# Kernel optimization log

Hardware: AMD Instinct MI355X
Metric: run time of the kernel (lower is better)

The kernel has to match this reference:

```python
import jax, jax.numpy as jnp
import numpy as np

B, T, H, IN, OUT, HORIZON = 65536, 15, 128, 6, 3, 10
LN_EPS = 1e-5


def _w(k, shape, s=0.08):
    return jax.random.normal(k, shape, jnp.float32) * s


def setup_inputs() -> dict:
    key = jax.random.key(0)
    ks = jax.random.split(key, 16)
    return {
        "x": jax.random.normal(ks[0], (B, T, IN), jnp.float32),
        # encoder layer 0 (input 6 -> 128), PyTorch LSTM gate order i,f,g,o
        "W_ih0": _w(ks[1], (4 * H, IN)), "W_hh0": _w(ks[2], (4 * H, H)), "b0": jnp.zeros((4 * H,), jnp.float32),
        # encoder layer 1 (128 -> 128)
        "W_ih1": _w(ks[3], (4 * H, H)), "W_hh1": _w(ks[4], (4 * H, H)), "b1": jnp.zeros((4 * H,), jnp.float32),
        # decoder LSTM (128 -> 128)
        "W_ihd": _w(ks[5], (4 * H, H)), "W_hhd": _w(ks[6], (4 * H, H)), "bd": jnp.zeros((4 * H,), jnp.float32),
        # step embedding [pred_horizon+1, H]
        "emb": _w(ks[7], (HORIZON + 1, H), 0.5),
        # decoder_input_proj: Linear(3+128 -> 128)
        "Wp": _w(ks[8], (H, OUT + H)), "bp": jnp.zeros((H,), jnp.float32),
        # heads
        "Wm": _w(ks[9], (OUT, H)), "bm": jnp.zeros((OUT,), jnp.float32),
        "Ws": _w(ks[10], (OUT, H)), "bs": jnp.zeros((OUT,), jnp.float32),
        # dec_ln
        "ln_g": jnp.ones((H,), jnp.float32), "ln_b": jnp.zeros((H,), jnp.float32),
    }


def _lstm_cell(h, c, x_t, Wih, Whh, b):
    g = x_t @ Wih.T + h @ Whh.T + b  # [B, 4H]
    i, f, gg, o = jnp.split(g, 4, axis=-1)
    c = jax.nn.sigmoid(f) * c + jax.nn.sigmoid(i) * jnp.tanh(gg)
    h = jax.nn.sigmoid(o) * jnp.tanh(c)
    return h, c


def _run_lstm_layer(seq, Wih, Whh, b):
    # seq: [B, T, D] -> outputs [B, T, H], final (h, c)
    n = seq.shape[0]
    h0 = jnp.zeros((n, H), seq.dtype)
    c0 = jnp.zeros((n, H), seq.dtype)

    def step(carry, xt):
        h, c = carry
        h, c = _lstm_cell(h, c, xt, Wih, Whh, b)
        return (h, c), h

    (h, c), outs = jax.lax.scan(step, (h0, c0), jnp.swapaxes(seq, 0, 1))
    return jnp.swapaxes(outs, 0, 1), h, c


def _layernorm(x, g, b):
    mu = jnp.mean(x, axis=-1, keepdims=True)
    var = jnp.mean(jnp.square(x - mu), axis=-1, keepdims=True)
    return (x - mu) * jax.lax.rsqrt(var + LN_EPS) * g + b


def reference(x, W_ih0, W_hh0, b0, W_ih1, W_hh1, b1, W_ihd, W_hhd, bd, emb, Wp, bp, Wm, bm, Ws, bs, ln_g, ln_b):
    # --- encoder: 2-layer LSTM (eval mode, no dropout) ---
    out0, _, _ = _run_lstm_layer(x, W_ih0, W_hh0, b0)
    _, h_enc, c_enc = _run_lstm_layer(out0, W_ih1, W_hh1, b1)

    prev0 = x[:, -1, :OUT]  # [B, 3]
    n = x.shape[0]

    def dstep(carry, step):
        h, c, prev = carry
        se = jnp.broadcast_to(emb[step], (n, H))
        dec_in = jax.nn.relu(jnp.concatenate([prev, se], axis=-1) @ Wp.T + bp)
        h, c = _lstm_cell(h, c, dec_in, W_ihd, W_hhd, bd)
        feat = _layernorm(h, ln_g, ln_b)
        mu = feat @ Wm.T + bm
        ls = jnp.clip(feat @ Ws.T + bs, -6.0, 3.0)
        prev = jax.lax.stop_gradient(mu)  # mu.detach()
        return (h, c, prev), (mu, ls)

    _, (mus, lss) = jax.lax.scan(dstep, (h_enc, c_enc, prev0), jnp.arange(HORIZON))
    means = jnp.swapaxes(mus, 0, 1)     # [B, HORIZON, 3]
    log_stds = jnp.swapaxes(lss, 0, 1)  # [B, HORIZON, 3]
    return means, log_stds
```

## Files before the change

kernel.cpp:

```cpp
#include <hip/hip_runtime.h>
#include <stdint.h>

typedef __attribute__((ext_vector_type(8))) short short8;
typedef __attribute__((ext_vector_type(4))) float f32x4;

#define NT 15

#define SET0 0
#define SET1 81920
#define SET2 212992
#define SET3 344064
#define PK_TOTAL 346112
#define DBASE_OFF (PK_TOTAL*2)

__device__ __forceinline__ unsigned short f2bf(float f){
  unsigned int u = __builtin_bit_cast(unsigned int, f);
  u += 0x7fffu + ((u >> 16) & 1u);
  return (unsigned short)(u >> 16);
}
__device__ __forceinline__ float sigf(float x){
  return __builtin_amdgcn_rcpf(1.0f + __expf(-x));
}
__device__ __forceinline__ float tanhf_(float x){
  return 1.0f - 2.0f*__builtin_amdgcn_rcpf(1.0f + __expf(2.0f*x));
}
__device__ __forceinline__ int sidx(int row, int col){
  return row*128 + (col ^ ((row & 7) << 3));
}

__global__ void pack_w(const float* __restrict__ Wih0, const float* __restrict__ Whh0,
                       const float* __restrict__ Wih1, const float* __restrict__ Whh1,
                       const float* __restrict__ Wihd, const float* __restrict__ Whhd,
                       const float* __restrict__ Wm,  const float* __restrict__ Ws,
                       unsigned short* __restrict__ pk)
{
  int idx = blockIdx.x*256 + threadIdx.x;
  if (idx >= PK_TOTAL) return;
  float v = 0.f;
  if (idx >= SET3){
    int e = idx - SET3;
    int j = e & 7, lane = (e >> 3) & 63, kt = e >> 9;
    int n = lane & 15;
    int k = kt*32 + (lane >> 4)*8 + j;
    if (n < 3) v = Wm[n*128 + k];
    else if (n < 6) v = Ws[(n-3)*128 + k];
  } else {
    int set, e;
    if (idx < SET1){ set = 0; e = idx; }
    else if (idx < SET2){ set = 1; e = idx - SET1; }
    else { set = 2; e = idx - SET2; }
    int j = e & 7, lane = (e >> 3) & 63, rest = e >> 9;
    int nf = (set == 0) ? 5 : 8;
    int kt = rest % nf, pair = rest / nf;
    int g = pair & 3, jt = pair >> 2;
    int n = g*128 + jt*16 + (lane & 15);
    int kk = (lane >> 4)*8 + j;
    if (set == 0){
      if (kt < 4) v = Whh0[n*128 + kt*32 + kk];
      else if (kk < 6) v = Wih0[n*6 + kk];
    } else {
      const float* Wi = (set == 1) ? Wih1 : Wihd;
      const float* Wh = (set == 1) ? Whh1 : Whhd;
      v = (kt < 4) ? Wi[n*128 + kt*32 + kk] : Wh[n*128 + (kt-4)*32 + kk];
    }
  }
  pk[idx] = f2bf(v);
}

__global__ void prep_decbase(const float* __restrict__ emb, const float* __restrict__ Wp,
                             const float* __restrict__ bp, float* __restrict__ dbase)
{
  int idx = blockIdx.x*128 + threadIdx.x;
  if (idx >= 1280) return;
  int s = idx >> 7, j = idx & 127;
  float acc = bp[j];
  for (int k = 0; k < 128; ++k) acc += emb[s*128 + k] * Wp[j*131 + 3 + k];
  dbase[idx] = acc;
}

union DecShared {
  unsigned short xs[NT*64*8];
  struct {
    float sred[8][64][2];
    float mus[64][2];
    float prevb[64][4];
  } d;
};

__global__ __launch_bounds__(512)
void traj_main(const float* __restrict__ x,
               const unsigned short* __restrict__ pk,
               const float* __restrict__ dbase,
               const float* __restrict__ b0g, const float* __restrict__ b1g,
               const float* __restrict__ bdg,
               const float* __restrict__ Wp,
               const float* __restrict__ bm, const float* __restrict__ bs,
               const float* __restrict__ lng, const float* __restrict__ lnb,
               float* __restrict__ out)
{
  __shared__ __align__(16) unsigned short hA[2][64*128];
  __shared__ __align__(16) unsigned short hB[2][64*128];
  __shared__ __align__(16) DecShared u;

  const int tid  = threadIdx.x;
  const int w    = tid >> 6;
  const int lane = tid & 63;
  const int lidx = lane & 15;
  const int lgrp = lane >> 4;
  const int col  = w*16 + lidx;
  const int row0 = blockIdx.x * 64;

  for (int i = tid; i < 64*128; i += 512){ hA[0][i] = 0; hB[0][i] = 0; }
  for (int i = tid; i < NT*64*8; i += 512){
    int k8 = i & 7, r = (i >> 3) & 63, t = i >> 9;
    u.xs[i] = (k8 < 6) ? f2bf(x[(size_t)(row0 + r)*90 + t*6 + k8]) : (unsigned short)0;
  }

  float b0v[4], b1v[4];
  #pragma unroll
  for (int g = 0; g < 4; ++g){ b0v[g] = b0g[g*128 + col]; b1v[g] = b1g[g*128 + col]; }

  float c0[4][4], c1[4][4];
  #pragma unroll
  for (int m = 0; m < 4; ++m)
    #pragma unroll
    for (int r = 0; r < 4; ++r){ c0[m][r] = 0.f; c1[m][r] = 0.f; }

  __syncthreads();

  const unsigned short* pw0 = pk + SET0 + (w*4)*(5*512) + lane*8;
  const unsigned short* pw1 = pk + SET1 + (w*4)*(8*512) + lane*8;

  int ca = 0, cb = 0;
  #pragma unroll 1
  for (int t = 0; t < NT; ++t){
    short8 w0f[4][5];
    #pragma unroll
    for (int g = 0; g < 4; ++g)
      #pragma unroll
      for (int kt = 0; kt < 5; ++kt)
        w0f[g][kt] = *(const short8*)&pw0[(g*5 + kt)*512];
    #pragma unroll
    for (int m = 0; m < 4; ++m){
      const int arow = m*16 + lidx;
      short8 a[5];
      #pragma unroll
      for (int kt = 0; kt < 4; ++kt)
        a[kt] = *(const short8*)&hA[ca][sidx(arow, kt*32 + lgrp*8)];
      short8 ax = {0,0,0,0,0,0,0,0};
      if (lgrp == 0) ax = *(const short8*)&u.xs[(t*64 + arow)*8];
      a[4] = ax;
      f32x4 acc[4];
      #pragma unroll
      for (int g = 0; g < 4; ++g){
        f32x4 s = {0.f,0.f,0.f,0.f};
        #pragma unroll
        for (int kt = 0; kt < 5; ++kt)
          s = __builtin_amdgcn_mfma_f32_16x16x32_bf16(a[kt], w0f[g][kt], s, 0, 0, 0);
        acc[g] = s;
      }
      #pragma unroll
      for (int r = 0; r < 4; ++r){
        float iv = sigf(acc[0][r] + b0v[0]);
        float fv = sigf(acc[1][r] + b0v[1]);
        float gv = tanhf_(acc[2][r] + b0v[2]);
        float ov = sigf(acc[3][r] + b0v[3]);
        float c = fv*c0[m][r] + iv*gv;
        c0[m][r] = c;
        hA[ca^1][sidx(m*16 + lgrp*4 + r, col)] = f2bf(ov*tanhf_(c));
      }
    }
    __syncthreads();
    short8 w1f[4][8];
    #pragma unroll
    for (int g = 0; g < 4; ++g)
      #pragma unroll
      for (int kt = 0; kt < 8; ++kt)
        w1f[g][kt] = *(const short8*)&pw1[(g*8 + kt)*512];
    #pragma unroll
    for (int m = 0; m < 4; ++m){
      const int arow = m*16 + lidx;
      short8 a[8];
      #pragma unroll
      for (int kt = 0; kt < 4; ++kt)
        a[kt] = *(const short8*)&hA[ca^1][sidx(arow, kt*32 + lgrp*8)];
      #pragma unroll
      for (int kt = 0; kt < 4; ++kt)
        a[4+kt] = *(const short8*)&hB[cb][sidx(arow, kt*32 + lgrp*8)];
      f32x4 acc[4];
      #pragma unroll
      for (int g = 0; g < 4; ++g){
        f32x4 s = {0.f,0.f,0.f,0.f};
        #pragma unroll
        for (int kt = 0; kt < 8; ++kt)
          s = __builtin_amdgcn_mfma_f32_16x16x32_bf16(a[kt], w1f[g][kt], s, 0, 0, 0);
        acc[g] = s;
      }
      #pragma unroll
      for (int r = 0; r < 4; ++r){
        float iv = sigf(acc[0][r] + b1v[0]);
        float fv = sigf(acc[1][r] + b1v[1]);
        float gv = tanhf_(acc[2][r] + b1v[2]);
        float ov = sigf(acc[3][r] + b1v[3]);
        float c = fv*c1[m][r] + iv*gv;
        c1[m][r] = c;
        hB[cb^1][sidx(m*16 + lgrp*4 + r, col)] = f2bf(ov*tanhf_(c));
      }
    }
    __syncthreads();
    ca ^= 1; cb ^= 1;
  }

  const unsigned short* pw2 = pk + SET2 + (w*4)*(8*512) + lane*8;
  short8 wdf[4][8];
  #pragma unroll
  for (int g = 0; g < 4; ++g)
    #pragma unroll
    for (int kt = 0; kt < 8; ++kt)
      wdf[g][kt] = *(const short8*)&pw2[(g*8 + kt)*512];
  short8 whf[4];
  {
    const short8 z8 = {0,0,0,0,0,0,0,0};
    #pragma unroll
    for (int kt = 0; kt < 4; ++kt) whf[kt] = z8;
    if (w < 4){
      #pragma unroll
      for (int kt = 0; kt < 4; ++kt)
        whf[kt] = *(const short8*)&pk[SET3 + kt*512 + lane*8];
    }
  }

  const float wpa = Wp[col*131 + 0], wpb = Wp[col*131 + 1], wpc = Wp[col*131 + 2];
  const float lngv = lng[col], lnbv = lnb[col];
  float bdv[4];
  #pragma unroll
  for (int g = 0; g < 4; ++g) bdv[g] = bdg[g*128 + col];
  float bmo = 0.f;
  if (lidx < 3) bmo = bm[lidx];
  else if (lidx < 6) bmo = bs[lidx - 3];

  if (tid < 192){
    int r = tid / 3, o = tid - r*3;
    u.d.prevb[r][o] = x[(size_t)(row0 + r)*90 + 14*6 + o];
  }
  __syncthreads();

  int cbd = 1;
  #pragma unroll 1
  for (int s = 0; s < 10; ++s){
    const float dbs = dbase[s*128 + col];
    #pragma unroll
    for (int m = 0; m < 4; ++m)
      #pragma unroll
      for (int r = 0; r < 4; ++r){
        const int row = m*16 + lgrp*4 + r;
        f32x4 pv = *(const f32x4*)&u.d.prevb[row][0];
        float v = dbs + pv[0]*wpa + pv[1]*wpb + pv[2]*wpc;
        hA[0][sidx(row, col)] = f2bf(v > 0.f ? v : 0.f);
      }
    __syncthreads();

    float hv[4][4];
    #pragma unroll
    for (int m = 0; m < 4; ++m){
      const int arow = m*16 + lidx;
      short8 a[8];
      #pragma unroll
      for (int kt = 0; kt < 4; ++kt)
        a[kt] = *(const short8*)&hA[0][sidx(arow, kt*32 + lgrp*8)];
      #pragma unroll
      for (int kt = 0; kt < 4; ++kt)
        a[4+kt] = *(const short8*)&hB[cbd][sidx(arow, kt*32 + lgrp*8)];
      f32x4 acc[4];
      #pragma unroll
      for (int g = 0; g < 4; ++g){
        f32x4 sa = {0.f,0.f,0.f,0.f};
        #pragma unroll
        for (int kt = 0; kt < 8; ++kt)
          sa = __builtin_amdgcn_mfma_f32_16x16x32_bf16(a[kt], wdf[g][kt], sa, 0, 0, 0);
        acc[g] = sa;
      }
      #pragma unroll
      for (int r = 0; r < 4; ++r){
        float iv = sigf(acc[0][r] + bdv[0]);
        float fv = sigf(acc[1][r] + bdv[1]);
        float gv = tanhf_(acc[2][r] + bdv[2]);
        float ov = sigf(acc[3][r] + bdv[3]);
        float c = fv*c1[m][r] + iv*gv;
        c1[m][r] = c;
        float h = ov*tanhf_(c);
        hv[m][r] = h;
        hB[cbd^1][sidx(m*16 + lgrp*4 + r, col)] = f2bf(h);
      }
    }
    {
      float s1[4][4];
      #pragma unroll
      for (int m = 0; m < 4; ++m)
        #pragma unroll
        for (int r = 0; r < 4; ++r) s1[m][r] = hv[m][r];
      #pragma unroll
      for (int d = 1; d < 16; d <<= 1)
        #pragma unroll
        for (int m = 0; m < 4; ++m)
          #pragma unroll
          for (int r = 0; r < 4; ++r) s1[m][r] += __shfl_xor(s1[m][r], d);
      if (lidx == 0){
        #pragma unroll
        for (int m = 0; m < 4; ++m)
          #pragma unroll
          for (int r = 0; r < 4; ++r)
            u.d.sred[w][m*16 + lgrp*4 + r][0] = s1[m][r];
      }
      float s2[4][4];
      #pragma unroll
      for (int m = 0; m < 4; ++m)
        #pragma unroll
        for (int r = 0; r < 4; ++r) s2[m][r] = hv[m][r]*hv[m][r];
      #pragma unroll
      for (int d = 1; d < 16; d <<= 1)
        #pragma unroll
        for (int m = 0; m < 4; ++m)
          #pragma unroll
          for (int r = 0; r < 4; ++r) s2[m][r] += __shfl_xor(s2[m][r], d);
      if (lidx == 0){
        #pragma unroll
        for (int m = 0; m < 4; ++m)
          #pragma unroll
          for (int r = 0; r < 4; ++r)
            u.d.sred[w][m*16 + lgrp*4 + r][1] = s2[m][r];
      }
    }
    __syncthreads();
    if (tid < 64){
      float ss = 0.f, sq = 0.f;
      #pragma unroll
      for (int ww = 0; ww < 8; ++ww){ ss += u.d.sred[ww][tid][0]; sq += u.d.sred[ww][tid][1]; }
      float mu = ss * (1.f/128.f);
      float var = sq * (1.f/128.f) - mu*mu;
      u.d.mus[tid][0] = mu;
      u.d.mus[tid][1] = __builtin_amdgcn_rsqf(var + 1e-5f);
    }
    __syncthreads();
    #pragma unroll
    for (int m = 0; m < 4; ++m)
      #pragma unroll
      for (int r = 0; r < 4; ++r){
        const int row = m*16 + lgrp*4 + r;
        float mu = u.d.mus[row][0], rs = u.d.mus[row][1];
        hA[0][sidx(row, col)] = f2bf((hv[m][r] - mu)*rs*lngv + lnbv);
      }
    __syncthreads();
    if (w < 4){
      const int arow = w*16 + lidx;
      short8 a[4];
      #pragma unroll
      for (int kt = 0; kt < 4; ++kt)
        a[kt] = *(const short8*)&hA[0][sidx(arow, kt*32 + lgrp*8)];
      f32x4 acc = {0.f,0.f,0.f,0.f};
      #pragma unroll
      for (int kt = 0; kt < 4; ++kt)
        acc = __builtin_amdgcn_mfma_f32_16x16x32_bf16(a[kt], whf[kt], acc, 0, 0, 0);
      #pragma unroll
      for (int r = 0; r < 4; ++r){
        const int row = w*16 + lgrp*4 + r;
        float v = acc[r] + bmo;
        if (lidx < 3){
          out[(size_t)(row0 + row)*30 + s*3 + lidx] = v;
          u.d.prevb[row][lidx] = v;
        } else if (lidx < 6){
          out[(size_t)65536*30 + (size_t)(row0 + row)*30 + s*3 + (lidx - 3)] =
              fminf(fmaxf(v, -6.f), 3.f);
        }
      }
    }
    __syncthreads();
    cbd ^= 1;
  }
}

extern "C" void kernel_launch(void* const* d_in, const int* in_sizes, int n_in,
                              void* d_out, int out_size, void* d_ws, size_t ws_size,
                              hipStream_t stream)
{
  const float* x    = (const float*)d_in[0];
  const float* Wih0 = (const float*)d_in[1];
  const float* Whh0 = (const float*)d_in[2];
  const float* b0   = (const float*)d_in[3];
  const float* Wih1 = (const float*)d_in[4];
  const float* Whh1 = (const float*)d_in[5];
  const float* b1   = (const float*)d_in[6];
  const float* Wihd = (const float*)d_in[7];
  const float* Whhd = (const float*)d_in[8];
  const float* bd   = (const float*)d_in[9];
  const float* emb  = (const float*)d_in[10];
  const float* Wp   = (const float*)d_in[11];
  const float* bp   = (const float*)d_in[12];
  const float* Wm   = (const float*)d_in[13];
  const float* bm   = (const float*)d_in[14];
  const float* Ws   = (const float*)d_in[15];
  const float* bs   = (const float*)d_in[16];
  const float* lng  = (const float*)d_in[17];
  const float* lnb  = (const float*)d_in[18];

  unsigned short* pkw = (unsigned short*)d_ws;
  float* dbase = (float*)((char*)d_ws + DBASE_OFF);

  pack_w<<<(PK_TOTAL + 255)/256, 256, 0, stream>>>(Wih0, Whh0, Wih1, Whh1,
                                                   Wihd, Whhd, Wm, Ws, pkw);
  prep_decbase<<<10, 128, 0, stream>>>(emb, Wp, bp, dbase);
  traj_main<<<1024, 512, 0, stream>>>(x, pkw, dbase, b0, b1, bd, Wp,
                                      bm, bs, lng, lnb, (float*)d_out);
}
```

Before: 2.163 ms.

## Single-buffer LSTM hidden state in LDS to raise occupancy

Replaces the double-buffered hA/hB shared arrays with single buffers and stages x in two halves, roughly halving LDS use per block. The hidden-state fragments are read into registers and a barrier is placed before they are overwritten. Launch bounds now request 6 waves per SIMD so more blocks can be resident on each CU. In exchange each timestep gets extra __syncthreads barriers, more registers are held live, and the register cap may force spills.

```diff
diff --git a/kernel.cpp b/kernel.cpp
--- a/kernel.cpp
+++ b/kernel.cpp
@@ -79,7 +79,7 @@
 }
 
 union DecShared {
-  unsigned short xs[NT*64*8];
+  unsigned short xs[8*64*8];
   struct {
     float sred[8][64][2];
     float mus[64][2];
@@ -87,7 +87,7 @@
   } d;
 };
 
-__global__ __launch_bounds__(512)
+__global__ __launch_bounds__(512, 6)
 void traj_main(const float* __restrict__ x,
                const unsigned short* __restrict__ pk,
                const float* __restrict__ dbase,
@@ -98,8 +98,8 @@
                const float* __restrict__ lng, const float* __restrict__ lnb,
                float* __restrict__ out)
 {
-  __shared__ __align__(16) unsigned short hA[2][64*128];
-  __shared__ __align__(16) unsigned short hB[2][64*128];
+  __shared__ __align__(16) unsigned short hA[64*128];
+  __shared__ __align__(16) unsigned short hB[64*128];
   __shared__ __align__(16) DecShared u;
 
   const int tid  = threadIdx.x;
@@ -110,53 +110,66 @@
   const int col  = w*16 + lidx;
   const int row0 = blockIdx.x * 64;
 
-  for (int i = tid; i < 64*128; i += 512){ hA[0][i] = 0; hB[0][i] = 0; }
-  for (int i = tid; i < NT*64*8; i += 512){
-    int k8 = i & 7, r = (i >> 3) & 63, t = i >> 9;
-    u.xs[i] = (k8 < 6) ? f2bf(x[(size_t)(row0 + r)*90 + t*6 + k8]) : (unsigned short)0;
+  for (int i = tid; i < 64*128; i += 512){ hA[i] = 0; hB[i] = 0; }
+  for (int i = tid; i < 8*64*8; i += 512){
+    int k8 = i & 7, r = (i >> 3) & 63, tt = i >> 9;
+    u.xs[i] = (k8 < 6) ? f2bf(x[(size_t)(row0 + r)*90 + tt*6 + k8]) : (unsigned short)0;
   }
 
   float b0v[4], b1v[4];
   #pragma unroll
   for (int g = 0; g < 4; ++g){ b0v[g] = b0g[g*128 + col]; b1v[g] = b1g[g*128 + col]; }
 
-  float c0[4][4], c1[4][4];
+  float c0s[4][4], c1s[4][4];
   #pragma unroll
   for (int m = 0; m < 4; ++m)
     #pragma unroll
-    for (int r = 0; r < 4; ++r){ c0[m][r] = 0.f; c1[m][r] = 0.f; }
+    for (int r = 0; r < 4; ++r){ c0s[m][r] = 0.f; c1s[m][r] = 0.f; }
 
   __syncthreads();
 
   const unsigned short* pw0 = pk + SET0 + (w*4)*(5*512) + lane*8;
   const unsigned short* pw1 = pk + SET1 + (w*4)*(8*512) + lane*8;
 
-  int ca = 0, cb = 0;
   #pragma unroll 1
   for (int t = 0; t < NT; ++t){
+    if (t == 8){
+      for (int i = tid; i < 7*64*8; i += 512){
+        int k8 = i & 7, r = (i >> 3) & 63, tt = i >> 9;
+        u.xs[i] = (k8 < 6) ? f2bf(x[(size_t)(row0 + r)*90 + (8 + tt)*6 + k8])
+                           : (unsigned short)0;
+      }
+      __syncthreads();
+    }
+    const int tc = t & 7;
+
     short8 w0f[4][5];
     #pragma unroll
     for (int g = 0; g < 4; ++g)
       #pragma unroll
       for (int kt = 0; kt < 5; ++kt)
         w0f[g][kt] = *(const short8*)&pw0[(g*5 + kt)*512];
+
+    short8 aA[4][4];
+    #pragma unroll
+    for (int m = 0; m < 4; ++m)
+      #pragma unroll
+      for (int kt = 0; kt < 4; ++kt)
+        aA[m][kt] = *(const short8*)&hA[sidx(m*16 + lidx, kt*32 + lgrp*8)];
+    __syncthreads();
+
     #pragma unroll
     for (int m = 0; m < 4; ++m){
-      const int arow = m*16 + lidx;
-      short8 a[5];
-      #pragma unroll
-      for (int kt = 0; kt < 4; ++kt)
-        a[kt] = *(const short8*)&hA[ca][sidx(arow, kt*32 + lgrp*8)];
       short8 ax = {0,0,0,0,0,0,0,0};
-      if (lgrp == 0) ax = *(const short8*)&u.xs[(t*64 + arow)*8];
-      a[4] = ax;
+      if (lgrp == 0) ax = *(const short8*)&u.xs[(tc*64 + m*16 + lidx)*8];
       f32x4 acc[4];
       #pragma unroll
       for (int g = 0; g < 4; ++g){
         f32x4 s = {0.f,0.f,0.f,0.f};
         #pragma unroll
-        for (int kt = 0; kt < 5; ++kt)
-          s = __builtin_amdgcn_mfma_f32_16x16x32_bf16(a[kt], w0f[g][kt], s, 0, 0, 0);
+        for (int kt = 0; kt < 4; ++kt)
+          s = __builtin_amdgcn_mfma_f32_16x16x32_bf16(aA[m][kt], w0f[g][kt], s, 0, 0, 0);
+        s = __builtin_amdgcn_mfma_f32_16x16x32_bf16(ax, w0f[g][4], s, 0, 0, 0);
         acc[g] = s;
       }
       #pragma unroll
@@ -165,35 +178,43 @@
         float fv = sigf(acc[1][r] + b0v[1]);
         float gv = tanhf_(acc[2][r] + b0v[2]);
         float ov = sigf(acc[3][r] + b0v[3]);
-        float c = fv*c0[m][r] + iv*gv;
-        c0[m][r] = c;
-        hA[ca^1][sidx(m*16 + lgrp*4 + r, col)] = f2bf(ov*tanhf_(c));
-      }
-    }
-    __syncthreads();
+        float c = fv*c0s[m][r] + iv*gv;
+        c0s[m][r] = c;
+        hA[sidx(m*16 + lgrp*4 + r, col)] = f2bf(ov*tanhf_(c));
+      }
+    }
     short8 w1f[4][8];
     #pragma unroll
     for (int g = 0; g < 4; ++g)
       #pragma unroll
       for (int kt = 0; kt < 8; ++kt)
         w1f[g][kt] = *(const short8*)&pw1[(g*8 + kt)*512];
+    __syncthreads();
+
+    short8 aH[4][4];
+    #pragma unroll
+    for (int m = 0; m < 4; ++m)
+      #pragma unroll
+      for (int kt = 0; kt < 4; ++kt)
+        aH[m][kt] = *(const short8*)&hB[sidx(m*16 + lidx, kt*32 + lgrp*8)];
+    __syncthreads();
+
     #pragma unroll
     for (int m = 0; m < 4; ++m){
-      const int arow = m*16 + lidx;
-      short8 a[8];
-      #pragma unroll
-      for (int kt = 0; kt < 4; ++kt)
-        a[kt] = *(const short8*)&hA[ca^1][sidx(arow, kt*32 + lgrp*8)];
-      #pragma unroll
-      for (int kt = 0; kt < 4; ++kt)
-        a[4+kt] = *(const short8*)&hB[cb][sidx(arow, kt*32 + lgrp*8)];
+      short8 aI[4];
+      #pragma unroll
+      for (int kt = 0; kt < 4; ++kt)
+        aI[kt] = *(const short8*)&hA[sidx(m*16 + lidx, kt*32 + lgrp*8)];
       f32x4 acc[4];
       #pragma unroll
       for (int g = 0; g < 4; ++g){
         f32x4 s = {0.f,0.f,0.f,0.f};
         #pragma unroll
-        for (int kt = 0; kt < 8; ++kt)
-          s = __builtin_amdgcn_mfma_f32_16x16x32_bf16(a[kt], w1f[g][kt], s, 0, 0, 0);
+        for (int kt = 0; kt < 4; ++kt)
+          s = __builtin_amdgcn_mfma_f32_16x16x32_bf16(aI[kt], w1f[g][kt], s, 0, 0, 0);
+        #pragma unroll
+        for (int kt = 0; kt < 4; ++kt)
+          s = __builtin_amdgcn_mfma_f32_16x16x32_bf16(aH[m][kt], w1f[g][4+kt], s, 0, 0, 0);
         acc[g] = s;
       }
       #pragma unroll
@@ -202,13 +223,11 @@
         float fv = sigf(acc[1][r] + b1v[1]);
         float gv = tanhf_(acc[2][r] + b1v[2]);
         float ov = sigf(acc[3][r] + b1v[3]);
-        float c = fv*c1[m][r] + iv*gv;
-        c1[m][r] = c;
-        hB[cb^1][sidx(m*16 + lgrp*4 + r, col)] = f2bf(ov*tanhf_(c));
-      }
-    }
-    __syncthreads();
-    ca ^= 1; cb ^= 1;
+        float c = fv*c1s[m][r] + iv*gv;
+        c1s[m][r] = c;
+        hB[sidx(m*16 + lgrp*4 + r, col)] = f2bf(ov*tanhf_(c));
+      }
+    }
   }
 
   const unsigned short* pw2 = pk + SET2 + (w*4)*(8*512) + lane*8;
@@ -229,7 +248,6 @@
         whf[kt] = *(const short8*)&pk[SET3 + kt*512 + lane*8];
     }
   }
-
   const float wpa = Wp[col*131 + 0], wpb = Wp[col*131 + 1], wpc = Wp[col*131 + 2];
   const float lngv = lng[col], lnbv = lnb[col];
   float bdv[4];
@@ -245,7 +263,6 @@
   }
   __syncthreads();
 
-  int cbd = 1;
   #pragma unroll 1
   for (int s = 0; s < 10; ++s){
     const float dbs = dbase[s*128 + col];
@@ -256,28 +273,35 @@
         const int row = m*16 + lgrp*4 + r;
         f32x4 pv = *(const f32x4*)&u.d.prevb[row][0];
         float v = dbs + pv[0]*wpa + pv[1]*wpb + pv[2]*wpc;
-        hA[0][sidx(row, col)] = f2bf(v > 0.f ? v : 0.f);
-      }
+        hA[sidx(row, col)] = f2bf(v > 0.f ? v : 0.f);
+      }
+    __syncthreads();
+
+    short8 aH[4][4];
+    #pragma unroll
+    for (int m = 0; m < 4; ++m)
+      #pragma unroll
+      for (int kt = 0; kt < 4; ++kt)
+        aH[m][kt] = *(const short8*)&hB[sidx(m*16 + lidx, kt*32 + lgrp*8)];
     __syncthreads();
 
     float hv[4][4];
     #pragma unroll
     for (int m = 0; m < 4; ++m){
-      const int arow = m*16 + lidx;
-      short8 a[8];
-      #pragma unroll
-      for (int kt = 0; kt < 4; ++kt)
-        a[kt] = *(const short8*)&hA[0][sidx(arow, kt*32 + lgrp*8)];
-      #pragma unroll
-      for (int kt = 0; kt < 4; ++kt)
-        a[4+kt] = *(const short8*)&hB[cbd][sidx(arow, kt*32 + lgrp*8)];
+      short8 aI[4];
+      #pragma unroll
+      for (int kt = 0; kt < 4; ++kt)
+        aI[kt] = *(const short8*)&hA[sidx(m*16 + lidx, kt*32 + lgrp*8)];
       f32x4 acc[4];
       #pragma unroll
       for (int g = 0; g < 4; ++g){
         f32x4 sa = {0.f,0.f,0.f,0.f};
         #pragma unroll
-        for (int kt = 0; kt < 8; ++kt)
-          sa = __builtin_amdgcn_mfma_f32_16x16x32_bf16(a[kt], wdf[g][kt], sa, 0, 0, 0);
+        for (int kt = 0; kt < 4; ++kt)
+          sa = __builtin_amdgcn_mfma_f32_16x16x32_bf16(aI[kt], wdf[g][kt], sa, 0, 0, 0);
+        #pragma unroll
+        for (int kt = 0; kt < 4; ++kt)
+          sa = __builtin_amdgcn_mfma_f32_16x16x32_bf16(aH[m][kt], wdf[g][4+kt], sa, 0, 0, 0);
         acc[g] = sa;
       }
       #pragma unroll
@@ -286,49 +310,36 @@
         float fv = sigf(acc[1][r] + bdv[1]);
         float gv = tanhf_(acc[2][r] + bdv[2]);
         float ov = sigf(acc[3][r] + bdv[3]);
-        float c = fv*c1[m][r] + iv*gv;
-        c1[m][r] = c;
+        float c = fv*c1s[m][r] + iv*gv;
+        c1s[m][r] = c;
         float h = ov*tanhf_(c);
         hv[m][r] = h;
-        hB[cbd^1][sidx(m*16 + lgrp*4 + r, col)] = f2bf(h);
+        hB[sidx(m*16 + lgrp*4 + r, col)] = f2bf(h);
       }
     }
     {
-      float s1[4][4];
+      float s1[4][4], s2[4][4];
       #pragma unroll
       for (int m = 0; m < 4; ++m)
         #pragma unroll
-        for (int r = 0; r < 4; ++r) s1[m][r] = hv[m][r];
+        for (int r = 0; r < 4; ++r){ s1[m][r] = hv[m][r]; s2[m][r] = hv[m][r]*hv[m][r]; }
       #pragma unroll
       for (int d = 1; d < 16; d <<= 1)
         #pragma unroll
         for (int m = 0; m < 4; ++m)
           #pragma unroll
-          for (int r = 0; r < 4; ++r) s1[m][r] += __shfl_xor(s1[m][r], d);
+          for (int r = 0; r < 4; ++r){
+            s1[m][r] += __shfl_xor(s1[m][r], d);
+            s2[m][r] += __shfl_xor(s2[m][r], d);
+          }
       if (lidx == 0){
         #pragma unroll
         for (int m = 0; m < 4; ++m)
           #pragma unroll
-          for (int r = 0; r < 4; ++r)
+          for (int r = 0; r < 4; ++r){
             u.d.sred[w][m*16 + lgrp*4 + r][0] = s1[m][r];
-      }
-      float s2[4][4];
-      #pragma unroll
-      for (int m = 0; m < 4; ++m)
-        #pragma unroll
-        for (int r = 0; r < 4; ++r) s2[m][r] = hv[m][r]*hv[m][r];
-      #pragma unroll
-      for (int d = 1; d < 16; d <<= 1)
-        #pragma unroll
-        for (int m = 0; m < 4; ++m)
-          #pragma unroll
-          for (int r = 0; r < 4; ++r) s2[m][r] += __shfl_xor(s2[m][r], d);
-      if (lidx == 0){
-        #pragma unroll
-        for (int m = 0; m < 4; ++m)
-          #pragma unroll
-          for (int r = 0; r < 4; ++r)
             u.d.sred[w][m*16 + lgrp*4 + r][1] = s2[m][r];
+          }
       }
     }
     __syncthreads();
@@ -348,15 +359,14 @@
       for (int r = 0; r < 4; ++r){
         const int row = m*16 + lgrp*4 + r;
         float mu = u.d.mus[row][0], rs = u.d.mus[row][1];
-        hA[0][sidx(row, col)] = f2bf((hv[m][r] - mu)*rs*lngv + lnbv);
+        hA[sidx(row, col)] = f2bf((hv[m][r] - mu)*rs*lngv + lnbv);
       }
     __syncthreads();
     if (w < 4){
-      const int arow = w*16 + lidx;
       short8 a[4];
       #pragma unroll
       for (int kt = 0; kt < 4; ++kt)
-        a[kt] = *(const short8*)&hA[0][sidx(arow, kt*32 + lgrp*8)];
+        a[kt] = *(const short8*)&hA[sidx(w*16 + lidx, kt*32 + lgrp*8)];
       f32x4 acc = {0.f,0.f,0.f,0.f};
       #pragma unroll
       for (int kt = 0; kt < 4; ++kt)
@@ -375,7 +385,6 @@
       }
     }
     __syncthreads();
-    cbd ^= 1;
   }
 }
 
```

After: 8.382 ms. 3.87x slower.
